# Kernel tuning notes

Measured on AMD Instinct MI355X. Metric: run time of the kernel, lower is better.

The kernel has to match this reference:

```python
import jax, jax.numpy as jnp
import numpy as np

# HeteNet distribute_compute reference: per-agent expert id (hete_pick) selects one of
# E heterogeneous expert MLPs; tokens are gathered per expert, run through that expert's
# actor net, and scattered back into a padded [n_threads, n_agents, n_action] output.
# Here each expert is a 2-layer MLP (Net._act actor head approximation):
#   logits = relu(x @ W1[e] + b1[e]) @ W2[e] + b2[e]
# The dispatch/combine is expressed as dense per-expert compute + one-hot combine,
# which is the mathematically identical (mask-select) form of the gather/scatter.

T, N, D, H, A, E = 64, 64, 512, 512, 32, 15  # threads, agents, obs_dim(+addon), hidden, actions, experts


def setup_inputs() -> dict:
    key = jax.random.key(0)
    k0, k1, k2, k3 = jax.random.split(key, 4)
    obs = jax.random.normal(k0, (T, N, D), dtype=jnp.float32)
    hete_pick = jax.random.randint(k1, (T, N), 0, E)  # expert id per agent
    W1 = jax.random.normal(k2, (E, D, H), dtype=jnp.float32) * (1.0 / np.sqrt(D))
    b1 = jnp.zeros((E, H), dtype=jnp.float32)
    W2 = jax.random.normal(k3, (E, H, A), dtype=jnp.float32) * (1.0 / np.sqrt(H))
    b2 = jnp.zeros((E, A), dtype=jnp.float32)
    return {"obs": obs, "W1": W1, "b1": b1, "W2": W2, "b2": b2, "hete_pick": hete_pick}


def reference(obs, W1, b1, W2, b2, hete_pick):
    # per-expert dense forward: [E, T, N, H]
    h = jax.nn.relu(jnp.einsum('tnd,edh->etnh', obs, W1) + b1[:, None, None, :])
    logits = jnp.einsum('etnh,eha->etna', h, W2) + b2[:, None, None, :]  # [E,T,N,A]
    # combine: scatter each expert's rows back per mask (hete_pick == e)
    onehot = (hete_pick[None, :, :] == jnp.arange(E)[:, None, None]).astype(obs.dtype)  # [E,T,N]
    return jnp.einsum('etna,etn->tna', logits, onehot)  # [T,N,A]
```

## Files before the change

### kernel.cpp

```cpp
#include <hip/hip_runtime.h>
#include <stdint.h>

#define NTOK 4096
#define DDIM 512
#define HDIM 512
#define ADIM 32
#define NEXP 15
#define TILE_M 32
#define GRID_M 288

typedef __attribute__((ext_vector_type(8))) short bf16x8;
typedef __attribute__((ext_vector_type(8))) unsigned short ushort8;
typedef __attribute__((ext_vector_type(4))) unsigned short ushort4v;
typedef __attribute__((ext_vector_type(4))) float f32x4;

__device__ __forceinline__ unsigned short f2bf(float f) {
  unsigned int u = __float_as_uint(f);
  u += 0x7fffu + ((u >> 16) & 1u);
  return (unsigned short)(u >> 16);
}

__device__ __forceinline__ void gld_lds16(const void* g, void* l) {
  __builtin_amdgcn_global_load_lds(
      (const __attribute__((address_space(1))) void*)g,
      (__attribute__((address_space(3))) void*)l, 16, 0, 0);
}

__global__ __launch_bounds__(256) void prep_kernel(
    const float* __restrict__ W1, const float* __restrict__ W2,
    unsigned short* __restrict__ W1I, unsigned short* __restrict__ W2T,
    float* __restrict__ out)
{
  extern __shared__ char smem[];
  const int bid = blockIdx.x;
  const int tid = threadIdx.x;
  const int x = bid & 7, s = bid >> 3;
  int role, e = 0, kc = 0;
  if (x < 7)       { role = 0; e = 2 * x + (s >> 4); kc = s & 15; }
  else if (s < 16) { role = 0; e = 14; kc = s; }
  else if (s < 31) { role = 1; e = s - 16; }
  else             { return; }

  if (role == 0) {
    float* sm = (float*)smem;
    const int r0 = kc * 32;
    const float* src = W1 + (size_t)e * (DDIM * HDIM) + (size_t)r0 * HDIM;
    #pragma unroll
    for (int v = 0; v < 16; ++v) {
      int i = v * 256 + tid;
      int row = i >> 7, col = (i & 127) * 4;
      *(float4*)(sm + row * 517 + col) = *(const float4*)(src + (size_t)row * 512 + col);
    }
    __syncthreads();
    unsigned short* dst = W1I + (size_t)(e * 16 + kc) * 512 * 32;
    const int p = tid & 3;
    #pragma unroll
    for (int w = 0; w < 8; ++w) {
      int n = w * 64 + (tid >> 2);
      int q = p ^ ((n >> 1) & 3);
      ushort8 vv;
      #pragma unroll
      for (int xx = 0; xx < 8; ++xx) vv[xx] = f2bf(sm[(q * 8 + xx) * 517 + n]);
      *(ushort8*)(dst + (size_t)n * 32 + p * 8) = vv;
    }
  } else {
    float4 z4; z4.x = 0.f; z4.y = 0.f; z4.z = 0.f; z4.w = 0.f;
    for (int i = e * 256 + tid; i < NTOK * ADIM / 4; i += 15 * 256)
      ((float4*)out)[i] = z4;
    float* sm = (float*)smem;
    const float* src = W2 + (size_t)e * (HDIM * ADIM);
    #pragma unroll
    for (int v = 0; v < 16; ++v) {
      int i = v * 256 + tid;
      int row = i >> 3, col = (i & 7) * 4;
      *(float4*)(sm + row * 36 + col) = *(const float4*)(src + (size_t)row * 32 + col);
    }
    __syncthreads();
    unsigned short* dst = W2T + (size_t)e * (ADIM * HDIM);
    const int a = tid >> 3, k0 = (tid & 7) * 64;
    #pragma unroll
    for (int w = 0; w < 8; ++w) {
      ushort8 vv;
      #pragma unroll
      for (int xx = 0; xx < 8; ++xx) vv[xx] = f2bf(sm[(size_t)(k0 + w * 8 + xx) * 36 + a]);
      *(ushort8*)(dst + (size_t)a * 512 + k0 + w * 8) = vv;
    }
  }
}

__global__ __launch_bounds__(256, 2) void moe_gemm(
    const float* __restrict__ obs, const float* __restrict__ b1,
    const float* __restrict__ b2, const int* __restrict__ pick,
    const unsigned short* __restrict__ W1I, const unsigned short* __restrict__ W2T,
    float* __restrict__ out)
{
  extern __shared__ char smem[];
  char* s_x = smem;
  char* wb0 = smem + 32768;
  char* wb1 = smem + 49152;
  char* wb2 = smem + 65536;
  int* s_wt   = (int*)wb2;
  int* s_we   = (int*)(wb2 + 256);
  int* s_list = (int*)(wb2 + 320);

  const int tid = threadIdx.x, lane = tid & 63, wave = tid >> 6;
  const int l15 = lane & 15, l4 = lane >> 4;

  int pk[16];
  {
    const int4* pv = (const int4*)pick + tid * 4;
    int4 q0 = pv[0], q1 = pv[1], q2 = pv[2], q3 = pv[3];
    pk[0]=q0.x; pk[1]=q0.y; pk[2]=q0.z; pk[3]=q0.w;
    pk[4]=q1.x; pk[5]=q1.y; pk[6]=q1.z; pk[7]=q1.w;
    pk[8]=q2.x; pk[9]=q2.y; pk[10]=q2.z; pk[11]=q2.w;
    pk[12]=q3.x; pk[13]=q3.y; pk[14]=q3.z; pk[15]=q3.w;
  }
  #pragma unroll
  for (int ee = 0; ee < NEXP; ++ee) {
    int v = 0;
    #pragma unroll
    for (int i = 0; i < 16; ++i) v += (pk[i] == ee) ? 1 : 0;
    #pragma unroll
    for (int off = 1; off < 64; off <<= 1) v += __shfl_xor(v, off, 64);
    if (lane == 0) s_wt[wave * 16 + ee] = v;
  }
  __syncthreads();
  int ntl[NEXP], ntiles = 0;
  #pragma unroll
  for (int ee = 0; ee < NEXP; ++ee) {
    int ct = s_wt[ee] + s_wt[16 + ee] + s_wt[32 + ee] + s_wt[48 + ee];
    ntl[ee] = (ct + TILE_M - 1) >> 5;
    ntiles += ntl[ee];
  }
  const int nphys = ntiles * 2;
  const int p = blockIdx.x;
  const int xq = nphys >> 3, xr = nphys & 7;
  const int xcd = p & 7, slot = p >> 3;
  const int cx = xq + (xcd < xr ? 1 : 0);
  if (slot >= cx) return;
  const int j2 = xcd * xq + (xcd < xr ? xcd : xr) + slot;
  const int jt = j2 >> 1, half = j2 & 1;
  int e = 0, til = 0, cnte = 0, cum = 0, found = 0;
  #pragma unroll
  for (int ee = 0; ee < NEXP; ++ee) {
    if (!found && jt < cum + ntl[ee]) {
      e = ee; til = jt - cum;
      cnte = s_wt[ee] + s_wt[16 + ee] + s_wt[32 + ee] + s_wt[48 + ee];
      found = 1;
    }
    cum += ntl[ee];
  }
  const int tile_lo = til * TILE_M;
  int mvalid = cnte - tile_lo; if (mvalid > TILE_M) mvalid = TILE_M;

  {
    int ce = 0;
    #pragma unroll
    for (int i = 0; i < 16; ++i) ce += (pk[i] == e) ? 1 : 0;
    int inc = ce;
    #pragma unroll
    for (int off = 1; off < 64; off <<= 1) {
      int v = __shfl_up(inc, off, 64);
      if (lane >= off) inc += v;
    }
    if (lane == 63) s_we[wave] = inc;
    __syncthreads();
    int base0 = 0;
    #pragma unroll
    for (int w = 0; w < 4; ++w) if (w < wave) base0 += s_we[w];
    int pos = base0 + inc - ce;
    #pragma unroll
    for (int i = 0; i < 16; ++i) {
      if (pk[i] == e) {
        int rel = pos - tile_lo;
        if (rel >= 0 && rel < TILE_M) s_list[rel] = tid * 16 + i;
        pos++;
      }
    }
  }
  __syncthreads();

  const int mt2 = wave >> 1, at2 = wave & 1;
  int tk[4];
  #pragma unroll
  for (int r = 0; r < 4; ++r) {
    int mrow = mt2 * 16 + l4 * 4 + r;
    tk[r] = s_list[mrow < mvalid ? mrow : 0];
  }

  const int nbl = wave * 64;
  const int hbase = half * 256;
  const unsigned short* w1i_e = W1I + (size_t)e * 16 * 512 * 32;
  const unsigned short* w2t_e = W2T + (size_t)e * (ADIM * HDIM);

  const int m = tid >> 3, s8 = tid & 7;
  const float* grow = obs + (size_t)s_list[m < mvalid ? m : mvalid - 1] * DDIM;
  float4 xf[16];
  #pragma unroll
  for (int si = 0; si < 8; ++si) {
    xf[si * 2]     = *(const float4*)(grow + (s8 + si * 8) * 8);
    xf[si * 2 + 1] = *(const float4*)(grow + (s8 + si * 8) * 8 + 4);
  }
  __builtin_amdgcn_sched_barrier(0);

  float4 bvv[4];
  #pragma unroll
  for (int nt = 0; nt < 4; ++nt)
    bvv[nt] = *(const float4*)(b1 + e * HDIM + hbase + nbl + nt * 16 + l4 * 4);
  __builtin_amdgcn_sched_barrier(0);

  auto issue_w1 = [&](int t, char* buf) {
    const unsigned short* wbase = w1i_e + (size_t)t * (512 * 32) + (size_t)hbase * 32;
    #pragma unroll
    for (int i = 0; i < 4; ++i) {
      int nb = nbl + i * 16;
      gld_lds16(wbase + (size_t)nb * 32 + lane * 8, buf + nb * 64);
    }
  };
  issue_w1(0, wb0);
  __builtin_amdgcn_sched_barrier(0);
  issue_w1(1, wb1);
  __builtin_amdgcn_sched_barrier(0);

  #pragma unroll
  for (int si = 0; si < 8; ++si) {
    int s = s8 + si * 8;
    float4 f0 = xf[si * 2], f1 = xf[si * 2 + 1];
    ushort8 v;
    v[0] = f2bf(f0.x); v[1] = f2bf(f0.y); v[2] = f2bf(f0.z); v[3] = f2bf(f0.w);
    v[4] = f2bf(f1.x); v[5] = f2bf(f1.y); v[6] = f2bf(f1.z); v[7] = f2bf(f1.w);
    *(ushort8*)(s_x + m * 1024 + ((s ^ (m & 7)) << 4)) = v;
  }
  __syncthreads();

  f32x4 acc[4][2];
  #pragma unroll
  for (int nt = 0; nt < 4; ++nt) {
    f32x4 b4 = {bvv[nt].x, bvv[nt].y, bvv[nt].z, bvv[nt].w};
    acc[nt][0] = b4; acc[nt][1] = b4;
  }

  #pragma unroll
  for (int t = 0; t < 16; ++t) {
    if (t < 14) {
      char* nxt = ((t + 2) % 3 == 0) ? wb0 : ((t + 2) % 3 == 1) ? wb1 : wb2;
      issue_w1(t + 2, nxt);
    } else if (t == 14) {
      #pragma unroll
      for (int i = 0; i < 4; ++i) {
        int o = wave * 4096 + i * 1024 + lane * 16;
        int a = o >> 9;
        int p16 = (o >> 4) & 31;
        gld_lds16(w2t_e + (size_t)a * 512 + hbase + (size_t)((p16 ^ (a & 7)) * 8),
                  wb1 + o);
      }
    }
    if (t < 15) asm volatile("s_waitcnt vmcnt(8)" ::: "memory");
    else        asm volatile("s_waitcnt vmcnt(4)" ::: "memory");
    __builtin_amdgcn_sched_barrier(0);

    const char* cw = (t % 3 == 0) ? wb0 : (t % 3 == 1) ? wb1 : wb2;
    bf16x8 wfr[4], xfr[2];
    #pragma unroll
    for (int nt = 0; nt < 4; ++nt) {
      int n = nbl + nt * 16 + l15;
      wfr[nt] = *(const bf16x8*)(cw + n * 64 + ((l4 ^ ((n >> 1) & 3)) << 4));
    }
    #pragma unroll
    for (int mt = 0; mt < 2; ++mt) {
      int mm = mt * 16 + l15;
      xfr[mt] = *(const bf16x8*)(s_x + mm * 1024 + ((((t << 2) + l4) ^ (mm & 7)) << 4));
    }
    #pragma unroll
    for (int nt = 0; nt < 4; ++nt)
      #pragma unroll
      for (int mt = 0; mt < 2; ++mt)
        acc[nt][mt] = __builtin_amdgcn_mfma_f32_16x16x32_bf16(wfr[nt], xfr[mt], acc[nt][mt], 0, 0, 0);
  }

  __syncthreads();

  #pragma unroll
  for (int nt = 0; nt < 4; ++nt) {
    int n0 = nbl + nt * 16 + l4 * 4;
    int sg = n0 >> 3, hsel = (n0 >> 2) & 1;
    #pragma unroll
    for (int mt = 0; mt < 2; ++mt) {
      int mm = mt * 16 + l15;
      ushort4v hv;
      #pragma unroll
      for (int r = 0; r < 4; ++r) hv[r] = f2bf(fmaxf(acc[nt][mt][r], 0.f));
      *(ushort4v*)(s_x + mm * 1024 + ((sg ^ (mm & 7)) << 4) + hsel * 8) = hv;
    }
  }
  __syncthreads();

  const int a2 = at2 * 16 + l15;
  float b2v = half ? 0.f : b2[e * ADIM + a2];
  f32x4 acc2 = {b2v, b2v, b2v, b2v};
  #pragma unroll
  for (int ks = 0; ks < 8; ++ks) {
    int mm = mt2 * 16 + l15;
    bf16x8 af = *(const bf16x8*)(s_x + mm * 1024 + ((((ks << 2) + l4) ^ (mm & 7)) << 4));
    bf16x8 bf = *(const bf16x8*)(wb1 + a2 * 512 + ((((ks << 2) + l4) ^ (a2 & 7)) << 4));
    acc2 = __builtin_amdgcn_mfma_f32_16x16x32_bf16(af, bf, acc2, 0, 0, 0);
  }
  #pragma unroll
  for (int r = 0; r < 4; ++r) {
    int mrow = mt2 * 16 + l4 * 4 + r;
    if (mrow < mvalid)
      atomicAdd(&out[(size_t)tk[r] * ADIM + a2], acc2[r]);
  }
}

__global__ __launch_bounds__(256) void naive_kernel(
    const float* __restrict__ obs, const float* __restrict__ W1,
    const float* __restrict__ b1, const float* __restrict__ W2,
    const float* __restrict__ b2, const int* __restrict__ pick,
    float* __restrict__ out)
{
  __shared__ float sx[DDIM];
  __shared__ float sh[HDIM];
  const int t = blockIdx.x, tid = threadIdx.x;
  const int e = pick[t];
  const float* x = obs + (size_t)t * DDIM;
  for (int i = tid; i < DDIM; i += 256) sx[i] = x[i];
  __syncthreads();
  const float* w1 = W1 + (size_t)e * DDIM * HDIM;
  for (int j = tid; j < HDIM; j += 256) {
    float a = b1[e * HDIM + j];
    for (int d = 0; d < DDIM; ++d) a = fmaf(sx[d], w1[(size_t)d * HDIM + j], a);
    sh[j] = a > 0.f ? a : 0.f;
  }
  __syncthreads();
  if (tid < ADIM) {
    const float* w2 = W2 + (size_t)e * HDIM * ADIM;
    float a = b2[e * ADIM + tid];
    for (int j = 0; j < HDIM; ++j) a = fmaf(sh[j], w2[(size_t)j * ADIM + tid], a);
    out[(size_t)t * ADIM + tid] = a;
  }
}

extern "C" void kernel_launch(void* const* d_in, const int* in_sizes, int n_in,
                              void* d_out, int out_size, void* d_ws, size_t ws_size,
                              hipStream_t stream)
{
  const float* obs = (const float*)d_in[0];
  const float* W1  = (const float*)d_in[1];
  const float* b1  = (const float*)d_in[2];
  const float* W2  = (const float*)d_in[3];
  const float* b2  = (const float*)d_in[4];
  const int* pick  = (const int*)d_in[5];
  float* out = (float*)d_out;
  (void)in_sizes; (void)n_in; (void)out_size;

  const size_t OFF_W1I   = 262144;
  const size_t OFF_W2T   = OFF_W1I + (size_t)NEXP * HDIM * DDIM * 2;
  const size_t WS_NEEDED = OFF_W2T + (size_t)NEXP * ADIM * HDIM * 2;

  if (ws_size < WS_NEEDED) {
    naive_kernel<<<dim3(NTOK), dim3(256), 0, stream>>>(obs, W1, b1, W2, b2, pick, out);
    return;
  }

  char* ws = (char*)d_ws;
  unsigned short* W1I = (unsigned short*)(ws + OFF_W1I);
  unsigned short* W2T = (unsigned short*)(ws + OFF_W2T);

  prep_kernel<<<dim3(256), dim3(256), 73728, stream>>>(W1, W2, W1I, W2T, out);
  moe_gemm<<<dim3(GRID_M), dim3(256), 81920, stream>>>(
      obs, b1, b2, pick, W1I, W2T, out);
}
```

Before: 30.50 us.

## Fuse weight conversion into single MoE kernel reading fp32 weights directly

```diff
diff --git a/kernel.cpp b/kernel.cpp
--- a/kernel.cpp
+++ b/kernel.cpp
@@ -7,11 +7,10 @@
 #define ADIM 32
 #define NEXP 15
 #define TILE_M 32
-#define GRID_M 288
+#define GRID_F 144
 
 typedef __attribute__((ext_vector_type(8))) short bf16x8;
 typedef __attribute__((ext_vector_type(8))) unsigned short ushort8;
-typedef __attribute__((ext_vector_type(4))) unsigned short ushort4v;
 typedef __attribute__((ext_vector_type(4))) float f32x4;
 
 __device__ __forceinline__ unsigned short f2bf(float f) {
@@ -20,88 +19,24 @@
   return (unsigned short)(u >> 16);
 }
 
-__device__ __forceinline__ void gld_lds16(const void* g, void* l) {
-  __builtin_amdgcn_global_load_lds(
-      (const __attribute__((address_space(1))) void*)g,
-      (__attribute__((address_space(3))) void*)l, 16, 0, 0);
-}
-
-__global__ __launch_bounds__(256) void prep_kernel(
-    const float* __restrict__ W1, const float* __restrict__ W2,
-    unsigned short* __restrict__ W1I, unsigned short* __restrict__ W2T,
+__device__ __forceinline__ bf16x8 pack8(const float* w) {
+  ushort8 v;
+  #pragma unroll
+  for (int j = 0; j < 8; ++j) v[j] = f2bf(w[j]);
+  union { ushort8 u; bf16x8 b; } cv; cv.u = v; return cv.b;
+}
+
+__global__ __launch_bounds__(256, 1) void hetenet_fused(
+    const float* __restrict__ obs, const float* __restrict__ W1,
+    const float* __restrict__ b1, const float* __restrict__ W2,
+    const float* __restrict__ b2, const int* __restrict__ pick,
     float* __restrict__ out)
 {
-  extern __shared__ char smem[];
-  const int bid = blockIdx.x;
-  const int tid = threadIdx.x;
-  const int x = bid & 7, s = bid >> 3;
-  int role, e = 0, kc = 0;
-  if (x < 7)       { role = 0; e = 2 * x + (s >> 4); kc = s & 15; }
-  else if (s < 16) { role = 0; e = 14; kc = s; }
-  else if (s < 31) { role = 1; e = s - 16; }
-  else             { return; }
-
-  if (role == 0) {
-    float* sm = (float*)smem;
-    const int r0 = kc * 32;
-    const float* src = W1 + (size_t)e * (DDIM * HDIM) + (size_t)r0 * HDIM;
-    #pragma unroll
-    for (int v = 0; v < 16; ++v) {
-      int i = v * 256 + tid;
-      int row = i >> 7, col = (i & 127) * 4;
-      *(float4*)(sm + row * 517 + col) = *(const float4*)(src + (size_t)row * 512 + col);
-    }
-    __syncthreads();
-    unsigned short* dst = W1I + (size_t)(e * 16 + kc) * 512 * 32;
-    const int p = tid & 3;
-    #pragma unroll
-    for (int w = 0; w < 8; ++w) {
-      int n = w * 64 + (tid >> 2);
-      int q = p ^ ((n >> 1) & 3);
-      ushort8 vv;
-      #pragma unroll
-      for (int xx = 0; xx < 8; ++xx) vv[xx] = f2bf(sm[(q * 8 + xx) * 517 + n]);
-      *(ushort8*)(dst + (size_t)n * 32 + p * 8) = vv;
-    }
-  } else {
-    float4 z4; z4.x = 0.f; z4.y = 0.f; z4.z = 0.f; z4.w = 0.f;
-    for (int i = e * 256 + tid; i < NTOK * ADIM / 4; i += 15 * 256)
-      ((float4*)out)[i] = z4;
-    float* sm = (float*)smem;
-    const float* src = W2 + (size_t)e * (HDIM * ADIM);
-    #pragma unroll
-    for (int v = 0; v < 16; ++v) {
-      int i = v * 256 + tid;
-      int row = i >> 3, col = (i & 7) * 4;
-      *(float4*)(sm + row * 36 + col) = *(const float4*)(src + (size_t)row * 32 + col);
-    }
-    __syncthreads();
-    unsigned short* dst = W2T + (size_t)e * (ADIM * HDIM);
-    const int a = tid >> 3, k0 = (tid & 7) * 64;
-    #pragma unroll
-    for (int w = 0; w < 8; ++w) {
-      ushort8 vv;
-      #pragma unroll
-      for (int xx = 0; xx < 8; ++xx) vv[xx] = f2bf(sm[(size_t)(k0 + w * 8 + xx) * 36 + a]);
-      *(ushort8*)(dst + (size_t)a * 512 + k0 + w * 8) = vv;
-    }
-  }
-}
-
-__global__ __launch_bounds__(256, 2) void moe_gemm(
-    const float* __restrict__ obs, const float* __restrict__ b1,
-    const float* __restrict__ b2, const int* __restrict__ pick,
-    const unsigned short* __restrict__ W1I, const unsigned short* __restrict__ W2T,
-    float* __restrict__ out)
-{
-  extern __shared__ char smem[];
-  char* s_x = smem;
-  char* wb0 = smem + 32768;
-  char* wb1 = smem + 49152;
-  char* wb2 = smem + 65536;
-  int* s_wt   = (int*)wb2;
-  int* s_we   = (int*)(wb2 + 256);
-  int* s_list = (int*)(wb2 + 320);
+  __shared__ char s_xraw[32768];
+  __shared__ int s_wt[4][16];
+  __shared__ int s_we[4];
+  __shared__ int s_list[TILE_M];
+  char* s_x = s_xraw;
 
   const int tid = threadIdx.x, lane = tid & 63, wave = tid >> 6;
   const int l15 = lane & 15, l4 = lane >> 4;
@@ -122,30 +57,28 @@
     for (int i = 0; i < 16; ++i) v += (pk[i] == ee) ? 1 : 0;
     #pragma unroll
     for (int off = 1; off < 64; off <<= 1) v += __shfl_xor(v, off, 64);
-    if (lane == 0) s_wt[wave * 16 + ee] = v;
+    if (lane == 0) s_wt[wave][ee] = v;
   }
   __syncthreads();
   int ntl[NEXP], ntiles = 0;
   #pragma unroll
   for (int ee = 0; ee < NEXP; ++ee) {
-    int ct = s_wt[ee] + s_wt[16 + ee] + s_wt[32 + ee] + s_wt[48 + ee];
+    int ct = s_wt[0][ee] + s_wt[1][ee] + s_wt[2][ee] + s_wt[3][ee];
     ntl[ee] = (ct + TILE_M - 1) >> 5;
     ntiles += ntl[ee];
   }
-  const int nphys = ntiles * 2;
   const int p = blockIdx.x;
-  const int xq = nphys >> 3, xr = nphys & 7;
+  const int xq = ntiles >> 3, xr = ntiles & 7;
   const int xcd = p & 7, slot = p >> 3;
   const int cx = xq + (xcd < xr ? 1 : 0);
   if (slot >= cx) return;
-  const int j2 = xcd * xq + (xcd < xr ? xcd : xr) + slot;
-  const int jt = j2 >> 1, half = j2 & 1;
+  const int jt = xcd * xq + (xcd < xr ? xcd : xr) + slot;
   int e = 0, til = 0, cnte = 0, cum = 0, found = 0;
   #pragma unroll
   for (int ee = 0; ee < NEXP; ++ee) {
     if (!found && jt < cum + ntl[ee]) {
       e = ee; til = jt - cum;
-      cnte = s_wt[ee] + s_wt[16 + ee] + s_wt[32 + ee] + s_wt[48 + ee];
+      cnte = s_wt[0][ee] + s_wt[1][ee] + s_wt[2][ee] + s_wt[3][ee];
       found = 1;
     }
     cum += ntl[ee];
@@ -180,91 +113,45 @@
   }
   __syncthreads();
 
-  const int mt2 = wave >> 1, at2 = wave & 1;
-  int tk[4];
-  #pragma unroll
-  for (int r = 0; r < 4; ++r) {
-    int mrow = mt2 * 16 + l4 * 4 + r;
-    tk[r] = s_list[mrow < mvalid ? mrow : 0];
-  }
-
-  const int nbl = wave * 64;
-  const int hbase = half * 256;
-  const unsigned short* w1i_e = W1I + (size_t)e * 16 * 512 * 32;
-  const unsigned short* w2t_e = W2T + (size_t)e * (ADIM * HDIM);
-
-  const int m = tid >> 3, s8 = tid & 7;
-  const float* grow = obs + (size_t)s_list[m < mvalid ? m : mvalid - 1] * DDIM;
-  float4 xf[16];
-  #pragma unroll
-  for (int si = 0; si < 8; ++si) {
-    xf[si * 2]     = *(const float4*)(grow + (s8 + si * 8) * 8);
-    xf[si * 2 + 1] = *(const float4*)(grow + (s8 + si * 8) * 8 + 4);
-  }
-  __builtin_amdgcn_sched_barrier(0);
-
-  float4 bvv[4];
-  #pragma unroll
-  for (int nt = 0; nt < 4; ++nt)
-    bvv[nt] = *(const float4*)(b1 + e * HDIM + hbase + nbl + nt * 16 + l4 * 4);
-  __builtin_amdgcn_sched_barrier(0);
-
-  auto issue_w1 = [&](int t, char* buf) {
-    const unsigned short* wbase = w1i_e + (size_t)t * (512 * 32) + (size_t)hbase * 32;
-    #pragma unroll
-    for (int i = 0; i < 4; ++i) {
-      int nb = nbl + i * 16;
-      gld_lds16(wbase + (size_t)nb * 32 + lane * 8, buf + nb * 64);
-    }
-  };
-  issue_w1(0, wb0);
-  __builtin_amdgcn_sched_barrier(0);
-  issue_w1(1, wb1);
-  __builtin_amdgcn_sched_barrier(0);
-
-  #pragma unroll
-  for (int si = 0; si < 8; ++si) {
-    int s = s8 + si * 8;
-    float4 f0 = xf[si * 2], f1 = xf[si * 2 + 1];
-    ushort8 v;
-    v[0] = f2bf(f0.x); v[1] = f2bf(f0.y); v[2] = f2bf(f0.z); v[3] = f2bf(f0.w);
-    v[4] = f2bf(f1.x); v[5] = f2bf(f1.y); v[6] = f2bf(f1.z); v[7] = f2bf(f1.w);
-    *(ushort8*)(s_x + m * 1024 + ((s ^ (m & 7)) << 4)) = v;
-  }
-  __syncthreads();
-
-  f32x4 acc[4][2];
-  #pragma unroll
-  for (int nt = 0; nt < 4; ++nt) {
-    f32x4 b4 = {bvv[nt].x, bvv[nt].y, bvv[nt].z, bvv[nt].w};
+  const float* W1e = W1 + (size_t)e * (DDIM * HDIM);
+  const float* W2e = W2 + (size_t)e * (HDIM * ADIM);
+  const int nbase = wave * 128;
+
+  {
+    const int m = tid >> 3, s8 = tid & 7;
+    const float* grow = obs + (size_t)s_list[m < mvalid ? m : mvalid - 1] * DDIM;
+    #pragma unroll
+    for (int si = 0; si < 8; ++si) {
+      int s = s8 + si * 8;
+      float4 f0 = *(const float4*)(grow + s * 8);
+      float4 f1 = *(const float4*)(grow + s * 8 + 4);
+      ushort8 v;
+      v[0] = f2bf(f0.x); v[1] = f2bf(f0.y); v[2] = f2bf(f0.z); v[3] = f2bf(f0.w);
+      v[4] = f2bf(f1.x); v[5] = f2bf(f1.y); v[6] = f2bf(f1.z); v[7] = f2bf(f1.w);
+      *(ushort8*)(s_x + m * 1024 + ((s ^ (m & 7)) << 4)) = v;
+    }
+  }
+  __syncthreads();
+
+  f32x4 acc[8][2];
+  #pragma unroll
+  for (int nt = 0; nt < 8; ++nt) {
+    float4 bv = *(const float4*)(b1 + e * HDIM + nbase + nt * 16 + l4 * 4);
+    f32x4 b4 = {bv.x, bv.y, bv.z, bv.w};
     acc[nt][0] = b4; acc[nt][1] = b4;
   }
 
   #pragma unroll
   for (int t = 0; t < 16; ++t) {
-    if (t < 14) {
-      char* nxt = ((t + 2) % 3 == 0) ? wb0 : ((t + 2) % 3 == 1) ? wb1 : wb2;
-      issue_w1(t + 2, nxt);
-    } else if (t == 14) {
+    const int k0 = t * 32 + l4 * 8;
+    bf16x8 wfr[8], xfr[2];
+    #pragma unroll
+    for (int nt = 0; nt < 8; ++nt) {
+      const float* wp = W1e + (size_t)k0 * HDIM + (nbase + nt * 16 + l15);
+      float w[8];
       #pragma unroll
-      for (int i = 0; i < 4; ++i) {
-        int o = wave * 4096 + i * 1024 + lane * 16;
-        int a = o >> 9;
-        int p16 = (o >> 4) & 31;
-        gld_lds16(w2t_e + (size_t)a * 512 + hbase + (size_t)((p16 ^ (a & 7)) * 8),
-                  wb1 + o);
-      }
-    }
-    if (t < 15) asm volatile("s_waitcnt vmcnt(8)" ::: "memory");
-    else        asm volatile("s_waitcnt vmcnt(4)" ::: "memory");
-    __builtin_amdgcn_sched_barrier(0);
-
-    const char* cw = (t % 3 == 0) ? wb0 : (t % 3 == 1) ? wb1 : wb2;
-    bf16x8 wfr[4], xfr[2];
-    #pragma unroll
-    for (int nt = 0; nt < 4; ++nt) {
-      int n = nbl + nt * 16 + l15;
-      wfr[nt] = *(const bf16x8*)(cw + n * 64 + ((l4 ^ ((n >> 1) & 3)) << 4));
+      for (int j = 0; j < 8; ++j) w[j] = wp[(size_t)j * HDIM];
+      wfr[nt] = pack8(w);
     }
     #pragma unroll
     for (int mt = 0; mt < 2; ++mt) {
@@ -272,7 +159,7 @@
       xfr[mt] = *(const bf16x8*)(s_x + mm * 1024 + ((((t << 2) + l4) ^ (mm & 7)) << 4));
     }
     #pragma unroll
-    for (int nt = 0; nt < 4; ++nt)
+    for (int nt = 0; nt < 8; ++nt)
       #pragma unroll
       for (int mt = 0; mt < 2; ++mt)
         acc[nt][mt] = __builtin_amdgcn_mfma_f32_16x16x32_bf16(wfr[nt], xfr[mt], acc[nt][mt], 0, 0, 0);
@@ -281,12 +168,13 @@
   __syncthreads();
 
   #pragma unroll
-  for (int nt = 0; nt < 4; ++nt) {
-    int n0 = nbl + nt * 16 + l4 * 4;
+  for (int nt = 0; nt < 8; ++nt) {
+    int n0 = nbase + nt * 16 + l4 * 4;
     int sg = n0 >> 3, hsel = (n0 >> 2) & 1;
     #pragma unroll
     for (int mt = 0; mt < 2; ++mt) {
       int mm = mt * 16 + l15;
+      typedef __attribute__((ext_vector_type(4))) unsigned short ushort4v;
       ushort4v hv;
       #pragma unroll
       for (int r = 0; r < 4; ++r) hv[r] = f2bf(fmaxf(acc[nt][mt][r], 0.f));
@@ -295,49 +183,27 @@
   }
   __syncthreads();
 
+  const int mt2 = wave >> 1, at2 = wave & 1;
   const int a2 = at2 * 16 + l15;
-  float b2v = half ? 0.f : b2[e * ADIM + a2];
+  const float b2v = b2[e * ADIM + a2];
   f32x4 acc2 = {b2v, b2v, b2v, b2v};
   #pragma unroll
-  for (int ks = 0; ks < 8; ++ks) {
+  for (int ks = 0; ks < 16; ++ks) {
+    const int k0 = ks * 32 + l4 * 8;
     int mm = mt2 * 16 + l15;
     bf16x8 af = *(const bf16x8*)(s_x + mm * 1024 + ((((ks << 2) + l4) ^ (mm & 7)) << 4));
-    bf16x8 bf = *(const bf16x8*)(wb1 + a2 * 512 + ((((ks << 2) + l4) ^ (a2 & 7)) << 4));
+    const float* wp = W2e + (size_t)k0 * ADIM + a2;
+    float w[8];
+    #pragma unroll
+    for (int j = 0; j < 8; ++j) w[j] = wp[(size_t)j * ADIM];
+    bf16x8 bf = pack8(w);
     acc2 = __builtin_amdgcn_mfma_f32_16x16x32_bf16(af, bf, acc2, 0, 0, 0);
   }
   #pragma unroll
   for (int r = 0; r < 4; ++r) {
     int mrow = mt2 * 16 + l4 * 4 + r;
     if (mrow < mvalid)
-      atomicAdd(&out[(size_t)tk[r] * ADIM + a2], acc2[r]);
-  }
-}
-
-__global__ __launch_bounds__(256) void naive_kernel(
-    const float* __restrict__ obs, const float* __restrict__ W1,
-    const float* __restrict__ b1, const float* __restrict__ W2,
-    const float* __restrict__ b2, const int* __restrict__ pick,
-    float* __restrict__ out)
-{
-  __shared__ float sx[DDIM];
-  __shared__ float sh[HDIM];
-  const int t = blockIdx.x, tid = threadIdx.x;
-  const int e = pick[t];
-  const float* x = obs + (size_t)t * DDIM;
-  for (int i = tid; i < DDIM; i += 256) sx[i] = x[i];
-  __syncthreads();
-  const float* w1 = W1 + (size_t)e * DDIM * HDIM;
-  for (int j = tid; j < HDIM; j += 256) {
-    float a = b1[e * HDIM + j];
-    for (int d = 0; d < DDIM; ++d) a = fmaf(sx[d], w1[(size_t)d * HDIM + j], a);
-    sh[j] = a > 0.f ? a : 0.f;
-  }
-  __syncthreads();
-  if (tid < ADIM) {
-    const float* w2 = W2 + (size_t)e * HDIM * ADIM;
-    float a = b2[e * ADIM + tid];
-    for (int j = 0; j < HDIM; ++j) a = fmaf(sh[j], w2[(size_t)j * ADIM + tid], a);
-    out[(size_t)t * ADIM + tid] = a;
+      out[(size_t)s_list[mrow] * ADIM + a2] = acc2[r];
   }
 }
 
@@ -352,22 +218,8 @@
   const float* b2  = (const float*)d_in[4];
   const int* pick  = (const int*)d_in[5];
   float* out = (float*)d_out;
-  (void)in_sizes; (void)n_in; (void)out_size;
-
-  const size_t OFF_W1I   = 262144;
-  const size_t OFF_W2T   = OFF_W1I + (size_t)NEXP * HDIM * DDIM * 2;
-  const size_t WS_NEEDED = OFF_W2T + (size_t)NEXP * ADIM * HDIM * 2;
-
-  if (ws_size < WS_NEEDED) {
-    naive_kernel<<<dim3(NTOK), dim3(256), 0, stream>>>(obs, W1, b1, W2, b2, pick, out);
-    return;
-  }
-
-  char* ws = (char*)d_ws;
-  unsigned short* W1I = (unsigned short*)(ws + OFF_W1I);
-  unsigned short* W2T = (unsigned short*)(ws + OFF_W2T);
-
-  prep_kernel<<<dim3(256), dim3(256), 73728, stream>>>(W1, W2, W1I, W2T, out);
-  moe_gemm<<<dim3(GRID_M), dim3(256), 81920, stream>>>(
-      obs, b1, b2, pick, W1I, W2T, out);
-}
+  (void)in_sizes; (void)n_in; (void)out_size; (void)d_ws; (void)ws_size;
+
+  hetenet_fused<<<dim3(GRID_F), dim3(256), 0, stream>>>(
+      obs, W1, b1, W2, b2, pick, out);
+}
```

Measured after the change: 38.13 us. +25.0%, slower.
